# Performance work log

Hardware: AMD Instinct MI355X
Metric: run time of the kernel (lower is better)

## Reference

```python
import jax, jax.numpy as jnp
import numpy as np

B = 64
E = 512          # latent_size / h_dim
H = 8            # num_heads
D = E // H       # head_dim
MAX_AGENTS = 254 # max(agents_per_sample) for the deterministic counts below
NEG = -1e9


def setup_inputs() -> dict:
    key = jax.random.key(0)
    k_x, k_wi, k_bi, k_wo, k_bo = jax.random.split(key, 5)
    # deterministic variable agent counts in [128, 254]; sum == 11531, max == 254
    agents = jnp.array([128 + (3 * i) % 129 for i in range(B)], dtype=jnp.int32)
    total = 11531
    att_in = jax.random.normal(k_x, (total, E), dtype=jnp.float32)
    # nn.MultiheadAttention params: packed in-proj [3E, E] + bias, out-proj [E, E] + bias
    w_in = jax.random.normal(k_wi, (3 * E, E), dtype=jnp.float32) * 0.02
    b_in = jax.random.normal(k_bi, (3 * E,), dtype=jnp.float32) * 0.02
    w_out = jax.random.normal(k_wo, (E, E), dtype=jnp.float32) * 0.02
    b_out = jax.random.normal(k_bo, (E,), dtype=jnp.float32) * 0.02
    return {"att_in": att_in, "w_in": w_in, "b_in": b_in,
            "w_out": w_out, "b_out": b_out, "agents_per_sample": agents}


def reference(att_in, w_in, b_in, w_out, b_out, agents_per_sample):
    S = MAX_AGENTS
    # scatter packed rows into padded [B, S, E] via a clipped gather (jit-safe)
    offsets = jnp.cumsum(agents_per_sample) - agents_per_sample      # [B]
    pos = jnp.arange(S, dtype=jnp.int32)
    mask = pos[None, :] < agents_per_sample[:, None]                 # [B, S] valid
    idx = jnp.clip(offsets[:, None] + pos[None, :], 0, att_in.shape[0] - 1)
    padded = jnp.where(mask[..., None], att_in[idx], 0.0)            # [B, S, E]

    # fused QKV projection (torch packed in_proj), dropout disabled (eval)
    qkv = padded @ w_in.T + b_in                                     # [B, S, 3E]
    q, k, v = jnp.split(qkv, 3, axis=-1)
    q = q.reshape(B, S, H, D)
    k = k.reshape(B, S, H, D)
    v = v.reshape(B, S, H, D)

    scores = jnp.einsum('bqhd,bkhd->bhqk', q, k) * (D ** -0.5)      # [B, H, S, S]
    scores = jnp.where(mask[:, None, None, :], scores, NEG)          # key_padding_mask
    attn = jax.nn.softmax(scores, axis=-1)
    ctx = jnp.einsum('bhqk,bkhd->bqhd', attn, v).reshape(B, S, E)
    out = ctx @ w_out.T + b_out                                      # [B, S, E]
    # torch returns only valid rows per sample; zero the padded rows instead
    return out * mask[..., None]
```

## Files before the change

### kernel.cpp

```cpp
#include <hip/hip_runtime.h>
#include <hip/hip_bf16.h>

typedef __attribute__((ext_vector_type(8))) short bf16x8;
typedef __attribute__((ext_vector_type(4))) float f32x4;
typedef __attribute__((ext_vector_type(4))) int i32x4;
typedef __attribute__((ext_vector_type(4))) unsigned short u16x4;
typedef __attribute__((ext_vector_type(2))) unsigned ui2;
typedef __attribute__((ext_vector_type(4))) float fl4;

struct __attribute__((packed)) u16x4u { u16x4 v; };

__device__ __forceinline__ f32x4 mfma16(bf16x8 a, bf16x8 b, f32x4 c) {
    return __builtin_amdgcn_mfma_f32_16x16x32_bf16(a, b, c, 0, 0, 0);
}

__device__ __forceinline__ unsigned short f2b(float f) {
    unsigned u = __float_as_uint(f);
    unsigned r = (u + 0x7FFF + ((u >> 16) & 1)) >> 16;
    return (unsigned short)r;
}

__device__ __forceinline__ int bsearch_off(const int* s_off, int m) {
    int lo = 0, hi = 63;
    while (lo < hi) {
        int mid = (lo + hi + 1) >> 1;
        if (s_off[mid] <= m) lo = mid; else hi = mid - 1;
    }
    return lo;
}

__device__ __forceinline__ void gld_lds16(const __hip_bfloat16* g, __hip_bfloat16* l) {
    __builtin_amdgcn_global_load_lds(
        (const __attribute__((address_space(1))) void*)g,
        (__attribute__((address_space(3))) void*)l,
        16, 0, 0);
}

__global__ void k_prep(const unsigned short* __restrict__ src,
                       const void* __restrict__ b_in, const void* __restrict__ b_out,
                       const int* __restrict__ agents,
                       int* __restrict__ flag, int* __restrict__ offs,
                       float* __restrict__ bfi, float* __restrict__ bfo) {
    __shared__ int sh[256];
    __shared__ int sa[64];
    __shared__ int sflag;
    int tid = threadIdx.x;
    int h = 0;
    for (int i = tid; i < 16384; i += 256) {
        unsigned e = (src[i] >> 7) & 0xFF;
        if (e == 0xFF) h = 1;
    }
    sh[tid] = h;
    if (tid < 64) sa[tid] = agents[tid];
    __syncthreads();
    if (tid < 64) {
        int v = sh[tid] | sh[tid + 64] | sh[tid + 128] | sh[tid + 192];
        unsigned long long m = __ballot(v != 0);
        if (tid == 0) { flag[0] = (m != 0) ? 1 : 0; sflag = (m != 0) ? 1 : 0; }
        int ex = 0;
        for (int i = 0; i < 64; ++i) { int w = sa[i]; if (i < tid) ex += w; }
        offs[tid] = ex;
        if (tid == 63) offs[64] = ex + sa[63];
    }
    __syncthreads();
    int f = sflag;
    for (int i = tid; i < 1536; i += 256)
        bfi[i] = f ? ((const float*)b_in)[i]
                   : __bfloat162float(((const __hip_bfloat16*)b_in)[i]);
    for (int i = tid; i < 512; i += 256)
        bfo[i] = f ? ((const float*)b_out)[i]
                   : __bfloat162float(((const __hip_bfloat16*)b_out)[i]);
}

__global__ void k_cast_all(const void* __restrict__ sA, unsigned short* __restrict__ dA, int nA,
                           const void* __restrict__ sWi, unsigned short* __restrict__ dWi, int nWi,
                           const void* __restrict__ sWo, unsigned short* __restrict__ dWo, int nWo,
                           const int* __restrict__ flag) {
    int i = (blockIdx.x * 256 + threadIdx.x) * 4;
    const void* src; unsigned short* dst; int k;
    if (i < nA)            { src = sA;  dst = dA;  k = i; }
    else if (i < nA + nWi) { src = sWi; dst = dWi; k = i - nA; }
    else if (i < nA + nWi + nWo) { src = sWo; dst = dWo; k = i - nA - nWi; }
    else return;
    u16x4 o;
    if (flag[0]) {
        fl4 v = *(const fl4*)((const float*)src + k);
        o[0] = f2b(v[0]); o[1] = f2b(v[1]); o[2] = f2b(v[2]); o[3] = f2b(v[3]);
    } else {
        o = *(const u16x4*)((const unsigned short*)src + k);
    }
    *(u16x4*)(dst + k) = o;
}

template<int LDA, bool MROWS>
__device__ __forceinline__ void gemm_core(
    const __hip_bfloat16* __restrict__ A,
    const __hip_bfloat16* __restrict__ W,
    int m0, int n0, int total,
    __hip_bfloat16* As, __hip_bfloat16* Ws,
    f32x4 acc[4][4], int tid)
{
    int lane = tid & 63, quad = lane >> 4, c = lane & 15;
    int wave = tid >> 6;
    int wr = wave >> 1, wc = wave & 1;

    const __hip_bfloat16* gA[4];
    const __hip_bfloat16* gW[4];
    __hip_bfloat16* lA[4];
    __hip_bfloat16* lW[4];
#pragma unroll
    for (int j = 0; j < 4; ++j) {
        int L = j * 256 + tid;
        int row = L >> 3;
        int gseg = (L & 7) ^ (row & 7);
        int ar = m0 + row; if (ar > total - 1) ar = total - 1;
        gA[j] = A + (size_t)ar * LDA + gseg * 8;
        gW[j] = W + (size_t)(n0 + row) * 512 + gseg * 8;
        lA[j] = As + (size_t)(j * 256 + wave * 64) * 8;
        lW[j] = Ws + (size_t)(j * 256 + wave * 64) * 8;
    }

#pragma unroll
    for (int j = 0; j < 4; ++j) gld_lds16(gA[j], lA[j]);
#pragma unroll
    for (int j = 0; j < 4; ++j) gld_lds16(gW[j], lW[j]);

#pragma unroll
    for (int s = 0; s < 8; ++s) {
        const int cur = s & 1;
        const int nxt = cur ^ 1;
        if (s < 7) {
            int k0 = (s + 1) * 64;
#pragma unroll
            for (int j = 0; j < 4; ++j) gld_lds16(gA[j] + k0, lA[j] + nxt * (128 * 64));
#pragma unroll
            for (int j = 0; j < 4; ++j) gld_lds16(gW[j] + k0, lW[j] + nxt * (128 * 64));
            asm volatile("s_waitcnt vmcnt(8)" ::: "memory");
        } else {
            asm volatile("s_waitcnt vmcnt(0)" ::: "memory");
        }
        __builtin_amdgcn_s_barrier();
        const __hip_bfloat16* Ab = As + cur * (128 * 64);
        const __hip_bfloat16* Wb = Ws + cur * (128 * 64);
#pragma unroll
        for (int h = 0; h < 2; ++h) {
            bf16x8 af[4], wf[4];
#pragma unroll
            for (int t = 0; t < 4; ++t) {
                int rowa = wr * 64 + t * 16 + c;
                int rowb = wc * 64 + t * 16 + c;
                int ks = quad + 4 * h;
                af[t] = *(const bf16x8*)(Ab + (size_t)rowa * 64 + ((ks ^ (rowa & 7)) * 8));
                wf[t] = *(const bf16x8*)(Wb + (size_t)rowb * 64 + ((ks ^ (rowb & 7)) * 8));
            }
#pragma unroll
            for (int i = 0; i < 4; ++i)
#pragma unroll
                for (int j = 0; j < 4; ++j)
                    acc[i][j] = MROWS ? mfma16(af[i], wf[j], acc[i][j])
                                      : mfma16(wf[j], af[i], acc[i][j]);
        }
        if (s < 7) __builtin_amdgcn_s_barrier();
    }
}

__global__ __launch_bounds__(256) void k_qkv(
    const __hip_bfloat16* __restrict__ A,
    const __hip_bfloat16* __restrict__ W,
    const float* __restrict__ bias,
    const int* __restrict__ offs,
    __hip_bfloat16* __restrict__ qP,
    __hip_bfloat16* __restrict__ kP,
    __hip_bfloat16* __restrict__ vT,
    int total, int MT)
{
    __shared__ __hip_bfloat16 As[2 * 128 * 64];
    __shared__ __hip_bfloat16 Ws[2 * 128 * 64];
    __shared__ int s_off[65];
    int l = blockIdx.x;
    int inner = l >> 3;
    int cb = inner % 12;
    int rb = (l & 7) + 8 * (inner / 12);
    if (rb >= MT) return;
    int n0 = cb * 128;
    int m0 = rb * 128;
    int tid = threadIdx.x;
    if (tid < 65) s_off[tid] = offs[tid];
    int lane = tid & 63, quad = lane >> 4, c = lane & 15;
    int wave = tid >> 6, wr = wave >> 1, wc = wave & 1;
    f32x4 z = {0.f, 0.f, 0.f, 0.f};
    f32x4 acc[4][4] = {{z,z,z,z},{z,z,z,z},{z,z,z,z},{z,z,z,z}};

    if (n0 < 1024) {
        gemm_core<512, false>(A, W, m0, n0, total, As, Ws, acc, tid);
        __hip_bfloat16* dst = (n0 < 512) ? qP : kP;
        int nb = n0 & 511;
        int head = (nb + wc * 64) >> 6;
        fl4 bv4[4];
#pragma unroll
        for (int j = 0; j < 4; ++j)
            bv4[j] = *(const fl4*)&bias[n0 + wc * 64 + j * 16 + quad * 4];
#pragma unroll
        for (int i = 0; i < 4; ++i) {
            int m = m0 + wr * 64 + i * 16 + c;
            if (m >= total) continue;
            int lo = bsearch_off(s_off, m);
            int vs = m - s_off[lo];
            size_t rowp = ((size_t)(lo * 8 + head) * 256 + vs) * 64;
#pragma unroll
            for (int j = 0; j < 4; ++j) {
                int dcol = j * 16 + quad * 4;
                u16x4 o;
#pragma unroll
                for (int r = 0; r < 4; ++r) o[r] = f2b(acc[i][j][r] + bv4[j][r]);
                *(u16x4*)&dst[rowp + dcol] = o;
            }
        }
    } else {
        gemm_core<512, true>(A, W, m0, n0, total, As, Ws, acc, tid);
        float bv[4];
#pragma unroll
        for (int j = 0; j < 4; ++j) bv[j] = bias[n0 + wc * 64 + j * 16 + c];
#pragma unroll
        for (int i = 0; i < 4; ++i) {
            int m_base = m0 + wr * 64 + i * 16 + quad * 4;
            if (m_base >= total) continue;
            int lo = bsearch_off(s_off, m_base);
            bool vec = (m_base + 3 < total) && (s_off[lo + 1] > m_base + 3);
            if (vec) {
                int vs = m_base - s_off[lo];
#pragma unroll
                for (int j = 0; j < 4; ++j) {
                    int vc = n0 - 1024 + wc * 64 + j * 16 + c;
                    size_t idx = ((size_t)(lo * 8 + (vc >> 6)) * 64 + (vc & 63)) * 256 + vs;
                    u16x4 o;
#pragma unroll
                    for (int r = 0; r < 4; ++r) o[r] = f2b(acc[i][j][r] + bv[j]);
                    ((u16x4u*)&vT[idx])->v = o;
                }
            } else {
#pragma unroll
                for (int r = 0; r < 4; ++r) {
                    int m = m_base + r;
                    if (m >= total) continue;
                    int lo2 = bsearch_off(s_off, m);
                    int vs2 = m - s_off[lo2];
#pragma unroll
                    for (int j = 0; j < 4; ++j) {
                        int vc = n0 - 1024 + wc * 64 + j * 16 + c;
                        vT[((size_t)(lo2 * 8 + (vc >> 6)) * 64 + (vc & 63)) * 256 + vs2] =
                            __float2bfloat16(acc[i][j][r] + bv[j]);
                    }
                }
            }
        }
    }
}

__global__ __launch_bounds__(256, 2) void k_attn(
    const __hip_bfloat16* __restrict__ qP,
    const __hip_bfloat16* __restrict__ kP,
    const __hip_bfloat16* __restrict__ vT,
    __hip_bfloat16* __restrict__ ctx,
    const int* __restrict__ agents,
    const int* __restrict__ offs)
{
    __shared__ __attribute__((aligned(16))) char Pl[4][16 * 80];
    int bh = blockIdx.x;
    int b = bh >> 3, h = bh & 7;
    int n = agents[b];
    int off = offs[b];
    int qtiles = (n + 15) >> 4;
    int stmax = (qtiles + 1) >> 1;
    int tid = threadIdx.x;
    int wave = tid >> 6, lane = tid & 63, quad = lane >> 4, c = lane & 15;
    const __hip_bfloat16* qbase = qP + (size_t)bh * 256 * 64;
    const __hip_bfloat16* kbase = kP + (size_t)bh * 256 * 64 + quad * 8;
    const __hip_bfloat16* vbase = vT + (size_t)bh * 64 * 256;
    char* Plw = &Pl[wave][0];

    bf16x8 qB[4][2];
    int nt = 0;
#pragma unroll
    for (int t = 0; t < 4; ++t) {
        int qt = wave + 4 * t;
        if (qt < qtiles) {
            nt = t + 1;
            int qr = qt * 16 + c; if (qr > n - 1) qr = n - 1;
            const __hip_bfloat16* qp = qbase + (size_t)qr * 64 + quad * 8;
            qB[t][0] = *(const bf16x8*)qp;
            qB[t][1] = *(const bf16x8*)(qp + 32);
        }
    }

    f32x4 z = {0.f, 0.f, 0.f, 0.f};
    f32x4 O[4][4] = {{z,z,z,z},{z,z,z,z},{z,z,z,z},{z,z,z,z}};
    float sm[4] = {0.f, 0.f, 0.f, 0.f};

    auto LK = [&](int st, bf16x8 kA[2][2], bf16x8 vA[4]) {
        int k0 = st * 32;
#pragma unroll
        for (int ti = 0; ti < 2; ++ti) {
            int kr = k0 + ti * 16 + c; if (kr > n - 1) kr = n - 1;
            const __hip_bfloat16* kp = kbase + (size_t)kr * 64;
            kA[ti][0] = *(const bf16x8*)kp;
            kA[ti][1] = *(const bf16x8*)(kp + 32);
        }
#pragma unroll
        for (int dt = 0; dt < 4; ++dt)
            vA[dt] = *(const bf16x8*)(vbase + (size_t)(dt * 16 + c) * 256 + k0 + quad * 8);
    };

    auto CMP = [&](int st, bf16x8 kA[2][2], bf16x8 vA[4]) {
        int k0 = st * 32;
#pragma unroll
        for (int t = 0; t < 4; ++t) {
            if (t < nt) {
#pragma unroll
                for (int ti = 0; ti < 2; ++ti) {
                    f32x4 s = mfma16(kA[ti][0], qB[t][0], z);
                    s = mfma16(kA[ti][1], qB[t][1], s);
                    int kbase_i = k0 + ti * 16 + quad * 4;
                    float p0 = (kbase_i + 0 < n) ? __expf(s[0] * 0.125f) : 0.f;
                    float p1 = (kbase_i + 1 < n) ? __expf(s[1] * 0.125f) : 0.f;
                    float p2 = (kbase_i + 2 < n) ? __expf(s[2] * 0.125f) : 0.f;
                    float p3 = (kbase_i + 3 < n) ? __expf(s[3] * 0.125f) : 0.f;
                    sm[t] += (p0 + p1) + (p2 + p3);
                    ui2 dw;
                    dw[0] = (unsigned)f2b(p0) | ((unsigned)f2b(p1) << 16);
                    dw[1] = (unsigned)f2b(p2) | ((unsigned)f2b(p3) << 16);
                    *(ui2*)(Plw + c * 80 + ti * 32 + quad * 8) = dw;
                }
                bf16x8 pB = *(const bf16x8*)(Plw + c * 80 + quad * 16);
#pragma unroll
                for (int dt = 0; dt < 4; ++dt)
                    O[t][dt] = mfma16(vA[dt], pB, O[t][dt]);
            }
        }
    };

    bf16x8 kA[2][2], vA[4], kB[2][2], vB[4], kC[2][2], vC[4];
    LK(0, kA, vA);
    if (1 < stmax) LK(1, kB, vB);
    for (int st = 0; st < stmax; st += 3) {
        if (st + 2 < stmax) LK(st + 2, kC, vC);
        CMP(st, kA, vA);
        if (st + 3 < stmax) LK(st + 3, kA, vA);
        if (st + 1 < stmax) CMP(st + 1, kB, vB);
        if (st + 4 < stmax) LK(st + 4, kB, vB);
        if (st + 2 < stmax) CMP(st + 2, kC, vC);
    }

#pragma unroll
    for (int t = 0; t < 4; ++t) {
        if (t < nt) {
            float v = sm[t];
            v += __shfl_xor(v, 16);
            v += __shfl_xor(v, 32);
            float iv = 1.0f / v;
            int q = (wave + 4 * t) * 16 + c;
            if (q < n) {
                size_t row = (size_t)(off + q) * 512 + h * 64;
#pragma unroll
                for (int dt = 0; dt < 4; ++dt) {
                    u16x4 o;
#pragma unroll
                    for (int r = 0; r < 4; ++r) o[r] = f2b(O[t][dt][r] * iv);
                    *(u16x4*)&ctx[row + dt * 16 + quad * 4] = o;
                }
            }
        }
    }
}

__global__ __launch_bounds__(256) void k_out(
    const __hip_bfloat16* __restrict__ A,
    const __hip_bfloat16* __restrict__ W,
    const float* __restrict__ bias,
    const int* __restrict__ offs,
    const int* __restrict__ agents,
    void* __restrict__ out,
    const int* __restrict__ flag,
    int total, int MT)
{
    __shared__ __hip_bfloat16 As[2 * 128 * 64];
    __shared__ __hip_bfloat16 Ws[2 * 128 * 64];
    __shared__ int s_off[65];
    int l = blockIdx.x;
    int MTpad = ((MT + 7) >> 3) << 3;
    int tid = threadIdx.x;
    if (l >= 4 * MTpad) {
        int b = l - 4 * MTpad;
        int n = agents[b];
        int esz = flag[0] ? 4 : 2;
        long long base = ((long long)b * 254 + n) * 512 * esz;
        long long bytes = (long long)(254 - n) * 512 * esz;
        for (long long i = (long long)tid * 16; i < bytes; i += (long long)256 * 16)
            *(i32x4*)((char*)out + base + i) = (i32x4){0, 0, 0, 0};
        return;
    }
    int inner = l >> 3;
    int cb = inner & 3;
    int rb = (l & 7) + 8 * (inner >> 2);
    if (rb >= MT) return;
    int n0 = cb * 128;
    int m0 = rb * 128;
    if (tid < 65) s_off[tid] = offs[tid];
    f32x4 z = {0.f, 0.f, 0.f, 0.f};
    f32x4 acc[4][4] = {{z,z,z,z},{z,z,z,z},{z,z,z,z},{z,z,z,z}};
    gemm_core<512, false>(A, W, m0, n0, total, As, Ws, acc, tid);

    int f32m = flag[0];
    int lane = tid & 63, quad = lane >> 4, c = lane & 15;
    int wave = tid >> 6, wr = wave >> 1, wc = wave & 1;
    fl4 bv4[4];
#pragma unroll
    for (int j = 0; j < 4; ++j)
        bv4[j] = *(const fl4*)&bias[n0 + wc * 64 + j * 16 + quad * 4];
#pragma unroll
    for (int i = 0; i < 4; ++i) {
        int m = m0 + wr * 64 + i * 16 + c;
        if (m >= total) continue;
        int lo = bsearch_off(s_off, m);
        int os_ = m - s_off[lo];
        size_t rowb = ((size_t)(lo * 254 + os_)) * 512;
#pragma unroll
        for (int j = 0; j < 4; ++j) {
            int col0 = n0 + wc * 64 + j * 16 + quad * 4;
            if (f32m) {
                fl4 o;
#pragma unroll
                for (int r = 0; r < 4; ++r) o[r] = acc[i][j][r] + bv4[j][r];
                *(fl4*)&((float*)out)[rowb + col0] = o;
            } else {
                u16x4 o;
#pragma unroll
                for (int r = 0; r < 4; ++r) o[r] = f2b(acc[i][j][r] + bv4[j][r]);
                *(u16x4*)&((__hip_bfloat16*)out)[rowb + col0] = o;
            }
        }
    }
}

extern "C" void kernel_launch(void* const* d_in, const int* in_sizes, int n_in,
                              void* d_out, int out_size, void* d_ws, size_t ws_size,
                              hipStream_t stream) {
    const void* att_in = d_in[0];
    const void* w_in   = d_in[1];
    const void* b_in   = d_in[2];
    const void* w_out  = d_in[3];
    const void* b_out  = d_in[4];
    const int* agents  = (const int*)d_in[5];
    int total = in_sizes[0] / 512;

    char* p = (char*)d_ws;
    int* flag  = (int*)p;                 p += 256;
    int* offs  = (int*)p;                 p += 512;
    float* bfi = (float*)p;               p += 1536 * 4;
    float* bfo = (float*)p;               p += 512 * 4;
    __hip_bfloat16* WinBf  = (__hip_bfloat16*)p;  p += (size_t)1536 * 512 * 2;
    __hip_bfloat16* WoutBf = (__hip_bfloat16*)p;  p += (size_t)512 * 512 * 2;
    __hip_bfloat16* Abf    = (__hip_bfloat16*)p;  p += (size_t)total * 512 * 2;
    __hip_bfloat16* qP     = (__hip_bfloat16*)p;  p += (size_t)512 * 256 * 64 * 2;
    __hip_bfloat16* kP     = (__hip_bfloat16*)p;  p += (size_t)512 * 256 * 64 * 2;
    __hip_bfloat16* vT     = (__hip_bfloat16*)p;  p += (size_t)512 * 64 * 256 * 2;
    __hip_bfloat16* ctx    = (__hip_bfloat16*)p;  p += (size_t)total * 512 * 2;

    int nA = total * 512, nWi = 1536 * 512, nWo = 512 * 512;
    int ntot = nA + nWi + nWo;

    k_prep<<<1, 256, 0, stream>>>((const unsigned short*)att_in, b_in, b_out,
                                  agents, flag, offs, bfi, bfo);
    k_cast_all<<<(ntot / 4 + 255) / 256, 256, 0, stream>>>(
        att_in, (unsigned short*)Abf, nA,
        w_in,   (unsigned short*)WinBf, nWi,
        w_out,  (unsigned short*)WoutBf, nWo, flag);

    int MT = (total + 127) / 128;
    int MTpad = ((MT + 7) / 8) * 8;
    k_qkv<<<12 * MTpad, 256, 0, stream>>>(Abf, WinBf, bfi, offs, qP, kP, vT, total, MT);
    k_attn<<<512, 256, 0, stream>>>(qP, kP, vT, ctx, agents, offs);
    k_out<<<4 * MTpad + 64, 256, 0, stream>>>(ctx, WoutBf, bfo, offs, agents,
                                              d_out, flag, total, MT);
}
```

Baseline: 173.0 us.

## Enlarge QKV GEMM tile to 256x256 with 512-thread blocks

Replaces the 128x128 QKV projection tile (256 threads, 4 waves) with a 256x256 tile computed by 8 waves, each producing a 128x64 sub-tile with 8x4 MFMA accumulators. The larger tile raises arithmetic intensity and cuts redundant global loads of A and W. The grid shrinks from 12*MTpad blocks to 6*ceil(total/256), and the grouped row-block rasterization is dropped. In exchange, registers per thread roughly double and LDS grows to 128 KB per block, which may limit occupancy (launch_bounds asks for 2 blocks per CU). The smaller grid (about 270 blocks) may also underfill the GPU's CUs.

```diff
diff --git a/kernel.cpp b/kernel.cpp
--- a/kernel.cpp
+++ b/kernel.cpp
@@ -164,7 +164,82 @@
     }
 }
 
-__global__ __launch_bounds__(256) void k_qkv(
+template<bool MROWS>
+__device__ __forceinline__ void gemm256_core(
+    const __hip_bfloat16* __restrict__ A,
+    const __hip_bfloat16* __restrict__ W,
+    int m0, int n0, int total,
+    __hip_bfloat16* As, __hip_bfloat16* Ws,
+    f32x4 acc[8][4], int tid)
+{
+    int lane = tid & 63, quad = lane >> 4, c = lane & 15;
+    int wave = tid >> 6;
+    int wm = wave >> 2, wn = wave & 3;
+
+    const __hip_bfloat16* gA[4];
+    const __hip_bfloat16* gW[4];
+    __hip_bfloat16* lA[4];
+    __hip_bfloat16* lW[4];
+#pragma unroll
+    for (int j = 0; j < 4; ++j) {
+        int L = j * 512 + tid;
+        int row = L >> 3;
+        int gseg = (L & 7) ^ (row & 7);
+        int ar = m0 + row; if (ar > total - 1) ar = total - 1;
+        gA[j] = A + (size_t)ar * 512 + gseg * 8;
+        gW[j] = W + (size_t)(n0 + row) * 512 + gseg * 8;
+        lA[j] = As + (size_t)(j * 512 + wave * 64) * 8;
+        lW[j] = Ws + (size_t)(j * 512 + wave * 64) * 8;
+    }
+
+#pragma unroll
+    for (int j = 0; j < 4; ++j) gld_lds16(gA[j], lA[j]);
+#pragma unroll
+    for (int j = 0; j < 4; ++j) gld_lds16(gW[j], lW[j]);
+
+#pragma unroll
+    for (int s = 0; s < 8; ++s) {
+        const int cur = s & 1;
+        const int nxt = cur ^ 1;
+        if (s < 7) {
+            int k0 = (s + 1) * 64;
+#pragma unroll
+            for (int j = 0; j < 4; ++j) gld_lds16(gA[j] + k0, lA[j] + nxt * (256 * 64));
+#pragma unroll
+            for (int j = 0; j < 4; ++j) gld_lds16(gW[j] + k0, lW[j] + nxt * (256 * 64));
+            asm volatile("s_waitcnt vmcnt(8)" ::: "memory");
+        } else {
+            asm volatile("s_waitcnt vmcnt(0)" ::: "memory");
+        }
+        __builtin_amdgcn_s_barrier();
+        const __hip_bfloat16* Ab = As + cur * (256 * 64);
+        const __hip_bfloat16* Wb = Ws + cur * (256 * 64);
+#pragma unroll
+        for (int h = 0; h < 2; ++h) {
+            bf16x8 af[8], wf[4];
+            int ks = quad + 4 * h;
+#pragma unroll
+            for (int t = 0; t < 8; ++t) {
+                int rowa = wm * 128 + t * 16 + c;
+                af[t] = *(const bf16x8*)(Ab + (size_t)rowa * 64 + ((ks ^ (rowa & 7)) * 8));
+            }
+#pragma unroll
+            for (int t = 0; t < 4; ++t) {
+                int rowb = wn * 64 + t * 16 + c;
+                wf[t] = *(const bf16x8*)(Wb + (size_t)rowb * 64 + ((ks ^ (rowb & 7)) * 8));
+            }
+#pragma unroll
+            for (int i = 0; i < 8; ++i)
+#pragma unroll
+                for (int j = 0; j < 4; ++j)
+                    acc[i][j] = MROWS ? mfma16(af[i], wf[j], acc[i][j])
+                                      : mfma16(wf[j], af[i], acc[i][j]);
+        }
+        if (s < 7) __builtin_amdgcn_s_barrier();
+    }
+}
+
+__global__ __launch_bounds__(512, 2) void k_qkv(
     const __hip_bfloat16* __restrict__ A,
     const __hip_bfloat16* __restrict__ W,
     const float* __restrict__ bias,
@@ -172,37 +247,36 @@
     __hip_bfloat16* __restrict__ qP,
     __hip_bfloat16* __restrict__ kP,
     __hip_bfloat16* __restrict__ vT,
-    int total, int MT)
+    int total)
 {
-    __shared__ __hip_bfloat16 As[2 * 128 * 64];
-    __shared__ __hip_bfloat16 Ws[2 * 128 * 64];
+    __shared__ __hip_bfloat16 As[2 * 256 * 64];
+    __shared__ __hip_bfloat16 Ws[2 * 256 * 64];
     __shared__ int s_off[65];
     int l = blockIdx.x;
-    int inner = l >> 3;
-    int cb = inner % 12;
-    int rb = (l & 7) + 8 * (inner / 12);
-    if (rb >= MT) return;
-    int n0 = cb * 128;
-    int m0 = rb * 128;
+    int rb = l / 6;
+    int cb = l - rb * 6;
+    int n0 = cb * 256;
+    int m0 = rb * 256;
     int tid = threadIdx.x;
     if (tid < 65) s_off[tid] = offs[tid];
     int lane = tid & 63, quad = lane >> 4, c = lane & 15;
-    int wave = tid >> 6, wr = wave >> 1, wc = wave & 1;
+    int wave = tid >> 6, wm = wave >> 2, wn = wave & 3;
     f32x4 z = {0.f, 0.f, 0.f, 0.f};
-    f32x4 acc[4][4] = {{z,z,z,z},{z,z,z,z},{z,z,z,z},{z,z,z,z}};
+    f32x4 acc[8][4] = {{z,z,z,z},{z,z,z,z},{z,z,z,z},{z,z,z,z},
+                       {z,z,z,z},{z,z,z,z},{z,z,z,z},{z,z,z,z}};
 
     if (n0 < 1024) {
-        gemm_core<512, false>(A, W, m0, n0, total, As, Ws, acc, tid);
+        gemm256_core<false>(A, W, m0, n0, total, As, Ws, acc, tid);
         __hip_bfloat16* dst = (n0 < 512) ? qP : kP;
         int nb = n0 & 511;
-        int head = (nb + wc * 64) >> 6;
+        int head = (nb + wn * 64) >> 6;
         fl4 bv4[4];
 #pragma unroll
         for (int j = 0; j < 4; ++j)
-            bv4[j] = *(const fl4*)&bias[n0 + wc * 64 + j * 16 + quad * 4];
-#pragma unroll
-        for (int i = 0; i < 4; ++i) {
-            int m = m0 + wr * 64 + i * 16 + c;
+            bv4[j] = *(const fl4*)&bias[n0 + wn * 64 + j * 16 + quad * 4];
+#pragma unroll
+        for (int i = 0; i < 8; ++i) {
+            int m = m0 + wm * 128 + i * 16 + c;
             if (m >= total) continue;
             int lo = bsearch_off(s_off, m);
             int vs = m - s_off[lo];
@@ -217,13 +291,13 @@
             }
         }
     } else {
-        gemm_core<512, true>(A, W, m0, n0, total, As, Ws, acc, tid);
+        gemm256_core<true>(A, W, m0, n0, total, As, Ws, acc, tid);
         float bv[4];
 #pragma unroll
-        for (int j = 0; j < 4; ++j) bv[j] = bias[n0 + wc * 64 + j * 16 + c];
-#pragma unroll
-        for (int i = 0; i < 4; ++i) {
-            int m_base = m0 + wr * 64 + i * 16 + quad * 4;
+        for (int j = 0; j < 4; ++j) bv[j] = bias[n0 + wn * 64 + j * 16 + c];
+#pragma unroll
+        for (int i = 0; i < 8; ++i) {
+            int m_base = m0 + wm * 128 + i * 16 + quad * 4;
             if (m_base >= total) continue;
             int lo = bsearch_off(s_off, m_base);
             bool vec = (m_base + 3 < total) && (s_off[lo + 1] > m_base + 3);
@@ -231,7 +305,7 @@
                 int vs = m_base - s_off[lo];
 #pragma unroll
                 for (int j = 0; j < 4; ++j) {
-                    int vc = n0 - 1024 + wc * 64 + j * 16 + c;
+                    int vc = n0 - 1024 + wn * 64 + j * 16 + c;
                     size_t idx = ((size_t)(lo * 8 + (vc >> 6)) * 64 + (vc & 63)) * 256 + vs;
                     u16x4 o;
 #pragma unroll
@@ -247,7 +321,7 @@
                     int vs2 = m - s_off[lo2];
 #pragma unroll
                     for (int j = 0; j < 4; ++j) {
-                        int vc = n0 - 1024 + wc * 64 + j * 16 + c;
+                        int vc = n0 - 1024 + wn * 64 + j * 16 + c;
                         vT[((size_t)(lo2 * 8 + (vc >> 6)) * 64 + (vc & 63)) * 256 + vs2] =
                             __float2bfloat16(acc[i][j][r] + bv[j]);
                     }
@@ -478,7 +552,8 @@
 
     int MT = (total + 127) / 128;
     int MTpad = ((MT + 7) / 8) * 8;
-    k_qkv<<<12 * MTpad, 256, 0, stream>>>(Abf, WinBf, bfi, offs, qP, kP, vT, total, MT);
+    int MT256 = (total + 255) / 256;
+    k_qkv<<<6 * MT256, 512, 0, stream>>>(Abf, WinBf, bfi, offs, qP, kP, vT, total);
     k_attn<<<512, 256, 0, stream>>>(qP, kP, vT, ctx, agents, offs);
     k_out<<<4 * MTpad + 64, 256, 0, stream>>>(ctx, WoutBf, bfo, offs, agents,
                                               d_out, flag, total, MT);
```

Result: slower. 190.2 us (+9.9%).
